# Kernel tuning notes

Hardware: AMD Instinct MI355X
Metric: run time of the kernel (lower is better)

The kernel has to match this reference:

```python
import jax, jax.numpy as jnp
import numpy as np

KERNEL_EPS = 1e-3   # generalized_kernel epsilon (performer)
Z_EPS = 1e-6        # LinearHopfieldCore eps


def _phi(x, proj):
    # generalized_kernel with relu: phi(x) = relu(d^{-0.25} * x @ P^T) + 1e-3
    # x: [B, L, H, D], proj: [M, D] -> [B, L, H, M]
    scale = x.shape[-1] ** -0.25
    return jax.nn.relu(jnp.einsum('blhd,md->blhm', x * scale, proj)) + KERNEL_EPS


def setup_inputs() -> dict:
    key = jax.random.key(0)
    kq, kk, kv, kp = jax.random.split(key, 4)
    B, L, H, D, M = 4, 4096, 16, 64, 256
    return {
        'q': jax.random.normal(kq, (B, L, H, D), dtype=jnp.float32),
        'k': jax.random.normal(kk, (B, L, H, D), dtype=jnp.float32),
        'v': jax.random.normal(kv, (B, L, H, D), dtype=jnp.float32),
        'projection_matrix': jax.random.normal(kp, (M, D), dtype=jnp.float32),
    }


def reference(q, k, v, projection_matrix):
    # Feature maps [B, L, H, M]
    Qf = _phi(q, projection_matrix)
    Kf = _phi(k, projection_matrix)
    # Linear attention (non-causal):
    # KV = sum_s K_s otimes V_s : [B, H, M, E]
    KV = jnp.einsum('bshm,bshe->bhme', Kf, v)
    # Z = 1 / (Q . (sum_s K_s + eps)) : [B, H, L]
    Ksum = jnp.sum(Kf, axis=1) + Z_EPS        # [B, H, M]
    Z = 1.0 / jnp.einsum('blhm,bhm->bhl', Qf, Ksum)
    # out = (Q @ KV) * Z : [B, L, H, E]
    out = jnp.einsum('bhme,blhm,bhl->blhe', KV, Qf, Z)
    return out
```

## Files before the change

kernel.cpp:

```cpp
#include <hip/hip_runtime.h>


#define LL 4096
#define HH 16
#define DD 64
#define EE 64
#define MM 256
#define SCALE 0.35355339059327378f

typedef __attribute__((ext_vector_type(8))) __bf16 bf8v;
typedef __attribute__((ext_vector_type(4))) __bf16 bf4v;
typedef __attribute__((ext_vector_type(4))) float f4v;

__device__ __forceinline__ __bf16 f2bf(float f) {
  union { float f; unsigned u; } x; x.f = f;
  unsigned r = (x.u + 0x7FFFu + ((x.u >> 16) & 1u)) >> 16;
  union { unsigned short s; __bf16 b; } y; y.s = (unsigned short)r;
  return y.b;
}

__device__ __forceinline__ void barrier_lgkm() {
  asm volatile("s_waitcnt lgkmcnt(0)" ::: "memory");
  __builtin_amdgcn_s_barrier();
  asm volatile("" ::: "memory");
}

#define MFMA16(a, b, c) __builtin_amdgcn_mfma_f32_16x16x32_bf16(a, b, c, 0, 0, 0)

#define PKV_ELEMS (8ull * 64 * 64 * 256)
#define PKS_ELEMS (8ull * 64 * 256)
#define KV_ELEMS (64ull * 64 * 256)
#define KS_ELEMS (64ull * 256)
#define WS_PART_BYTES ((PKV_ELEMS + PKS_ELEMS + KV_ELEMS + KS_ELEMS) * 4)
#define WS_ATOMIC_BYTES ((KV_ELEMS + KS_ELEMS) * 4)

#define ARENA_BYTES 72704
#define KT_OFF 0
#define VT_OFF 18432
#define KFT_OFF 35840

__global__ __launch_bounds__(512, 4)
void k1_kv(const float* __restrict__ kin, const float* __restrict__ vin,
           const float* __restrict__ pin,
           float* __restrict__ pkv, float* __restrict__ pks,
           float* __restrict__ kv, float* __restrict__ ks, int partials) {
  __shared__ alignas(16) char arena[ARENA_BYTES];
  __bf16* ktA[2] = {(__bf16*)(arena + KT_OFF), (__bf16*)(arena + KT_OFF) + 64 * 72};
  __bf16* vtA[2] = {(__bf16*)(arena + VT_OFF), (__bf16*)(arena + VT_OFF) + 64 * 68};
  __bf16* kft = (__bf16*)(arena + KFT_OFF);

  const int tid = threadIdx.x;
  const int w = tid >> 6;
  const int lane = tid & 63;
  const int qd = lane >> 4;
  const int nn = lane & 15;
  const int bh = blockIdx.y;
  const int b = bh >> 4, h = bh & 15;
  const int l0 = blockIdx.x * 512;

  const size_t bhbase = (size_t)b * LL * HH * DD + (size_t)h * DD;
  const int r0 = tid >> 4;
  const int c0 = (tid & 15) * 4;

  const float* gk = kin + bhbase + (size_t)(l0 + r0) * (HH * DD) + c0;
  const float* gv = vin + bhbase + (size_t)(l0 + r0) * (HH * DD) + c0;
  const size_t RSTEP = (size_t)32 * HH * DD;
  const size_t TSTEP = (size_t)64 * HH * DD;

  f4v kr[2][2], vr[2][2];
  kr[0][0] = *(const f4v*)gk;          kr[0][1] = *(const f4v*)(gk + RSTEP);
  vr[0][0] = *(const f4v*)gv;          vr[0][1] = *(const f4v*)(gv + RSTEP);
  gk += TSTEP; gv += TSTEP;
  kr[1][0] = *(const f4v*)gk;          kr[1][1] = *(const f4v*)(gk + RSTEP);
  vr[1][0] = *(const f4v*)gv;          vr[1][1] = *(const f4v*)(gv + RSTEP);
  gk += TSTEP; gv += TSTEP;

  bf8v pf[2][2];
#pragma unroll
  for (int mt = 0; mt < 2; ++mt) {
    const float* pr = pin + (size_t)(32 * w + mt * 16 + nn) * DD;
#pragma unroll
    for (int c = 0; c < 2; ++c) {
      bf8v t;
#pragma unroll
      for (int j = 0; j < 8; ++j) t[j] = f2bf(pr[c * 32 + qd * 8 + j] * SCALE);
      pf[mt][c] = t;
    }
  }

  f4v acc[2][4];
#pragma unroll
  for (int i = 0; i < 2; ++i)
#pragma unroll
    for (int j = 0; j < 4; ++j) acc[i][j] = (f4v){0.f, 0.f, 0.f, 0.f};
  float ksum[2] = {0.f, 0.f};

  auto stage = [&](int buf, const f4v* kk, const f4v* vv) {
    __bf16* ktb = ktA[buf];
    __bf16* vtb = vtA[buf];
#pragma unroll
    for (int rr = 0; rr < 2; ++rr) {
      bf4v a, c;
#pragma unroll
      for (int j = 0; j < 4; ++j) { a[j] = f2bf(kk[rr][j]); c[j] = f2bf(vv[rr][j]); }
      *(bf4v*)&ktb[(r0 + 32 * rr) * 72 + c0] = a;
      *(bf4v*)&vtb[(r0 + 32 * rr) * 68 + c0] = c;
    }
  };

  auto gemm12 = [&](int buf) {
    const __bf16* ktb = ktA[buf];
    const __bf16* vtb = vtA[buf];
#pragma unroll
    for (int lt = 0; lt < 4; ++lt) {
      bf8v a0 = *(const bf8v*)&ktb[(lt * 16 + nn) * 72 + qd * 8];
      bf8v a1 = *(const bf8v*)&ktb[(lt * 16 + nn) * 72 + 32 + qd * 8];
#pragma unroll
      for (int mt = 0; mt < 2; ++mt) {
        f4v cc = (f4v){0.f, 0.f, 0.f, 0.f};
        cc = MFMA16(a0, pf[mt][0], cc);
        cc = MFMA16(a1, pf[mt][1], cc);
        bf4v pk4;
#pragma unroll
        for (int r = 0; r < 4; ++r) {
          float ph = fmaxf(cc[r], 0.f) + 1e-3f;
          ksum[mt] += ph;
          pk4[r] = f2bf(ph);
        }
        *(bf4v*)&kft[(32 * w + mt * 16 + nn) * 72 + lt * 16 + qd * 4] = pk4;
      }
    }
#pragma unroll
    for (int c = 0; c < 2; ++c) {
      bf8v af0 = *(const bf8v*)&kft[(32 * w + nn) * 72 + c * 32 + qd * 8];
      bf8v af1 = *(const bf8v*)&kft[(32 * w + 16 + nn) * 72 + c * 32 + qd * 8];
#pragma unroll
      for (int et = 0; et < 4; ++et) {
        bf8v bv;
#pragma unroll
        for (int j = 0; j < 8; ++j) bv[j] = vtb[(c * 32 + qd * 8 + j) * 68 + et * 16 + nn];
        acc[0][et] = MFMA16(af0, bv, acc[0][et]);
        acc[1][et] = MFMA16(af1, bv, acc[1][et]);
      }
    }
  };

  stage(0, kr[0], vr[0]);
  barrier_lgkm();

#pragma unroll
  for (int t = 0; t < 8; ++t) {
    const int cur = t & 1;
    if (t + 2 < 8) {
      kr[cur][0] = *(const f4v*)gk;      kr[cur][1] = *(const f4v*)(gk + RSTEP);
      vr[cur][0] = *(const f4v*)gv;      vr[cur][1] = *(const f4v*)(gv + RSTEP);
      gk += TSTEP; gv += TSTEP;
    }
    gemm12(cur);
    if (t + 1 < 8) {
      stage(cur ^ 1, kr[cur ^ 1], vr[cur ^ 1]);
      barrier_lgkm();
    }
  }

  if (partials) {
    barrier_lgkm();
    float* ep = (float*)arena;
#pragma unroll
    for (int mt = 0; mt < 2; ++mt)
#pragma unroll
      for (int et = 0; et < 4; ++et)
        *(f4v*)&ep[(et * 16 + nn) * 260 + 32 * w + mt * 16 + 4 * qd] = acc[mt][et];
    barrier_lgkm();
    float* dst = pkv + (size_t)(blockIdx.x * 64 + bh) * (64 * 256);
#pragma unroll
    for (int rr = 0; rr < 8; ++rr) {
      int f = tid + 512 * rr;
      int e = f >> 6;
      int m4 = f & 63;
      f4v val = *(const f4v*)&ep[e * 260 + m4 * 4];
      ((f4v*)dst)[f] = val;
    }
#pragma unroll
    for (int mt = 0; mt < 2; ++mt) {
      float s = ksum[mt];
      s += __shfl_xor(s, 16, 64);
      s += __shfl_xor(s, 32, 64);
      if (lane < 16)
        pks[(size_t)(blockIdx.x * 64 + bh) * 256 + 32 * w + mt * 16 + lane] = s;
    }
  } else {
    float* kvb = kv + (size_t)bh * (64 * 256);
#pragma unroll
    for (int mt = 0; mt < 2; ++mt)
#pragma unroll
      for (int et = 0; et < 4; ++et)
#pragma unroll
        for (int r = 0; r < 4; ++r) {
          int m = 32 * w + mt * 16 + 4 * qd + r;
          int e = et * 16 + nn;
          atomicAdd(&kvb[e * 256 + m], acc[mt][et][r]);
        }
#pragma unroll
    for (int mt = 0; mt < 2; ++mt) {
      float s = ksum[mt];
      s += __shfl_xor(s, 16, 64);
      s += __shfl_xor(s, 32, 64);
      if (lane < 16) atomicAdd(&ks[bh * 256 + 32 * w + mt * 16 + lane], s);
    }
  }
}

__global__ __launch_bounds__(256)
void k2_red(const float* __restrict__ pkv, const float* __restrict__ pks,
            float* __restrict__ kv, float* __restrict__ ks) {
  const int idx = blockIdx.x * 256 + threadIdx.x;
  if (idx < 262144) {
    f4v s = (f4v){0.f, 0.f, 0.f, 0.f};
#pragma unroll
    for (int x = 0; x < 8; ++x) s += ((const f4v*)pkv)[(size_t)x * 262144 + idx];
    ((f4v*)kv)[idx] = s;
  } else {
    const int j = idx - 262144;
    f4v s = (f4v){0.f, 0.f, 0.f, 0.f};
#pragma unroll
    for (int x = 0; x < 8; ++x) s += ((const f4v*)pks)[x * 4096 + j];
    ((f4v*)ks)[j] = s;
  }
}

__global__ __launch_bounds__(512, 4)
void k3_out(const float* __restrict__ qin, const float* __restrict__ pin,
            const float* __restrict__ kv, const float* __restrict__ ksm,
            float* __restrict__ out) {
  __shared__ __bf16 qt[2][64 * 72];
  __shared__ __bf16 qf[64 * 264];
  __shared__ float denp[256];
  __shared__ float ksume[256];

  const int tid = threadIdx.x;
  const int w = tid >> 6;
  const int wm = w & 3;
  const int wl = w >> 2;
  const int lane = tid & 63;
  const int qd = lane >> 4;
  const int nn = lane & 15;
  const int bh = blockIdx.y;
  const int b = bh >> 4, h = bh & 15;
  const int l0 = blockIdx.x * 512;
  const int lt0 = 2 * wl;

  const size_t bhbase = (size_t)b * LL * HH * DD + (size_t)h * DD;
  const int r0 = tid >> 4;
  const int c0 = (tid & 15) * 4;

  const float* gq = qin + bhbase + (size_t)(l0 + r0) * (HH * DD) + c0;
  const size_t RSTEP = (size_t)32 * HH * DD;
  const size_t TSTEP = (size_t)64 * HH * DD;

  f4v qr[2][2];
  qr[0][0] = *(const f4v*)gq;  qr[0][1] = *(const f4v*)(gq + RSTEP);
  gq += TSTEP;
  qr[1][0] = *(const f4v*)gq;  qr[1][1] = *(const f4v*)(gq + RSTEP);
  gq += TSTEP;

  bf8v pf[4][2];
#pragma unroll
  for (int mt = 0; mt < 4; ++mt) {
    const float* pr = pin + (size_t)(64 * wm + mt * 16 + nn) * DD;
#pragma unroll
    for (int c = 0; c < 2; ++c) {
      bf8v t;
#pragma unroll
      for (int j = 0; j < 8; ++j) t[j] = f2bf(pr[c * 32 + qd * 8 + j] * SCALE);
      pf[mt][c] = t;
    }
  }

  const float* kvb = kv + (size_t)bh * (64 * 256);
  bf8v kvf[8];
#pragma unroll
  for (int c = 0; c < 8; ++c) {
    const float* src = kvb + (size_t)(16 * wm + nn) * 256 + c * 32 + qd * 8;
    bf8v t;
#pragma unroll
    for (int j = 0; j < 8; ++j) t[j] = f2bf(src[j]);
    kvf[c] = t;
  }

  if (tid < 256) ksume[tid] = ksm[bh * 256 + tid] + 1e-6f;

  auto stage = [&](int buf, const f4v* qq) {
    __bf16* qtb = &qt[buf][0];
#pragma unroll
    for (int rr = 0; rr < 2; ++rr) {
      bf4v a;
#pragma unroll
      for (int j = 0; j < 4; ++j) a[j] = f2bf(qq[rr][j]);
      *(bf4v*)&qtb[(r0 + 32 * rr) * 72 + c0] = a;
    }
  };

  stage(0, qr[0]);
  barrier_lgkm();

#pragma unroll
  for (int t = 0; t < 8; ++t) {
    const int cur = t & 1;
    if (t + 2 < 8) {
      qr[cur][0] = *(const f4v*)gq;  qr[cur][1] = *(const f4v*)(gq + RSTEP);
      gq += TSTEP;
    }

    {
      const __bf16* qtb = &qt[cur][0];
#pragma unroll
      for (int li = 0; li < 2; ++li) {
        const int lt = lt0 + li;
        bf8v b0 = *(const bf8v*)&qtb[(lt * 16 + nn) * 72 + qd * 8];
        bf8v b1 = *(const bf8v*)&qtb[(lt * 16 + nn) * 72 + 32 + qd * 8];
        float dpart = 0.f;
#pragma unroll
        for (int mt = 0; mt < 4; ++mt) {
          f4v cc = (f4v){0.f, 0.f, 0.f, 0.f};
          cc = MFMA16(pf[mt][0], b0, cc);
          cc = MFMA16(pf[mt][1], b1, cc);
          bf4v pk4;
#pragma unroll
          for (int r = 0; r < 4; ++r) {
            float ph = fmaxf(cc[r], 0.f) + 1e-3f;
            dpart += ph * ksume[64 * wm + mt * 16 + 4 * qd + r];
            pk4[r] = f2bf(ph);
          }
          *(bf4v*)&qf[(lt * 16 + nn) * 264 + 64 * wm + mt * 16 + 4 * qd] = pk4;
        }
        dpart += __shfl_xor(dpart, 16, 64);
        dpart += __shfl_xor(dpart, 32, 64);
        if (lane < 16) denp[wm * 64 + lt * 16 + lane] = dpart;
      }
    }
    barrier_lgkm();

#pragma unroll
    for (int li = 0; li < 2; ++li) {
      const int lt = lt0 + li;
      f4v co0 = (f4v){0.f, 0.f, 0.f, 0.f};
      f4v co1 = (f4v){0.f, 0.f, 0.f, 0.f};
#pragma unroll
      for (int c = 0; c < 4; ++c) {
        bf8v afa = *(const bf8v*)&qf[(lt * 16 + nn) * 264 + c * 32 + qd * 8];
        bf8v afb = *(const bf8v*)&qf[(lt * 16 + nn) * 264 + (c + 4) * 32 + qd * 8];
        co0 = MFMA16(afa, kvf[c], co0);
        co1 = MFMA16(afb, kvf[c + 4], co1);
      }
      f4v d0 = *(const f4v*)&denp[0 * 64 + lt * 16 + 4 * qd];
      f4v d1 = *(const f4v*)&denp[1 * 64 + lt * 16 + 4 * qd];
      f4v d2 = *(const f4v*)&denp[2 * 64 + lt * 16 + 4 * qd];
      f4v d3 = *(const f4v*)&denp[3 * 64 + lt * 16 + 4 * qd];
#pragma unroll
      for (int r = 0; r < 4; ++r) {
        int lrel = lt * 16 + 4 * qd + r;
        int labs = l0 + t * 64 + lrel;
        float rden = 1.f / (d0[r] + d1[r] + d2[r] + d3[r]);
        out[((size_t)((size_t)b * LL + labs) * HH + h) * EE + 16 * wm + nn] =
            (co0[r] + co1[r]) * rden;
      }
    }

    if (t + 1 < 8) {
      stage(cur ^ 1, qr[cur ^ 1]);
      barrier_lgkm();
    }
  }
}

extern "C" void kernel_launch(void* const* d_in, const int* in_sizes, int n_in,
                              void* d_out, int out_size, void* d_ws, size_t ws_size,
                              hipStream_t stream) {
  (void)in_sizes; (void)n_in; (void)out_size;
  const float* q = (const float*)d_in[0];
  const float* k = (const float*)d_in[1];
  const float* v = (const float*)d_in[2];
  const float* p = (const float*)d_in[3];
  float* ws = (float*)d_ws;
  float* out = (float*)d_out;

  dim3 grid(8, 64), blk(512);
  if (ws_size >= WS_PART_BYTES) {
    float* pkv = ws;
    float* pks = ws + PKV_ELEMS;
    float* kvp = ws + PKV_ELEMS + PKS_ELEMS;
    float* ksp = kvp + KV_ELEMS;
    k1_kv<<<grid, blk, 0, stream>>>(k, v, p, pkv, pks, nullptr, nullptr, 1);
    k2_red<<<dim3(1040), dim3(256), 0, stream>>>(pkv, pks, kvp, ksp);
    k3_out<<<grid, blk, 0, stream>>>(q, p, kvp, ksp, out);
  } else if (ws_size >= WS_ATOMIC_BYTES) {
    float* kvp = ws;
    float* ksp = ws + KV_ELEMS;
    hipMemsetAsync(d_ws, 0, WS_ATOMIC_BYTES, stream);
    k1_kv<<<grid, blk, 0, stream>>>(k, v, p, nullptr, nullptr, kvp, ksp, 0);
    k3_out<<<grid, blk, 0, stream>>>(q, p, kvp, ksp, out);
  }
}
```

Before: 376.5 us.

## Transpose V in LDS, pad rows to 76, hoist Ksum to registers, restage pipeline

In the KV kernel, V is now stored transposed in shared memory so the B-operand of the second MFMA is one vectorized 16-byte LDS read instead of eight strided scalar reads. Row strides change from 72/68/264 to 76/268 to shift bank-conflict patterns. Staging of the next tile now happens before the gemm with a single barrier per iteration, and the Q kernel keeps Ksum in registers instead of LDS. The custom bf16 rounding is replaced by the native cast, and occupancy hints drop from 4 to 3 blocks because of the larger LDS footprint.

```diff
diff --git a/kernel.cpp b/kernel.cpp
--- a/kernel.cpp
+++ b/kernel.cpp
@@ -12,12 +12,7 @@
 typedef __attribute__((ext_vector_type(4))) __bf16 bf4v;
 typedef __attribute__((ext_vector_type(4))) float f4v;
 
-__device__ __forceinline__ __bf16 f2bf(float f) {
-  union { float f; unsigned u; } x; x.f = f;
-  unsigned r = (x.u + 0x7FFFu + ((x.u >> 16) & 1u)) >> 16;
-  union { unsigned short s; __bf16 b; } y; y.s = (unsigned short)r;
-  return y.b;
-}
+__device__ __forceinline__ __bf16 f2bf(float f) { return (__bf16)f; }
 
 __device__ __forceinline__ void barrier_lgkm() {
   asm volatile("s_waitcnt lgkmcnt(0)" ::: "memory");
@@ -34,19 +29,19 @@
 #define WS_PART_BYTES ((PKV_ELEMS + PKS_ELEMS + KV_ELEMS + KS_ELEMS) * 4)
 #define WS_ATOMIC_BYTES ((KV_ELEMS + KS_ELEMS) * 4)
 
-#define ARENA_BYTES 72704
+#define ARENA_BYTES 77824
 #define KT_OFF 0
-#define VT_OFF 18432
-#define KFT_OFF 35840
-
-__global__ __launch_bounds__(512, 4)
+#define VT_OFF 19456
+#define KFT_OFF 38912
+
+__global__ __launch_bounds__(512, 3)
 void k1_kv(const float* __restrict__ kin, const float* __restrict__ vin,
            const float* __restrict__ pin,
            float* __restrict__ pkv, float* __restrict__ pks,
            float* __restrict__ kv, float* __restrict__ ks, int partials) {
   __shared__ alignas(16) char arena[ARENA_BYTES];
-  __bf16* ktA[2] = {(__bf16*)(arena + KT_OFF), (__bf16*)(arena + KT_OFF) + 64 * 72};
-  __bf16* vtA[2] = {(__bf16*)(arena + VT_OFF), (__bf16*)(arena + VT_OFF) + 64 * 68};
+  __bf16* ktA[2] = {(__bf16*)(arena + KT_OFF), (__bf16*)(arena + KT_OFF) + 64 * 76};
+  __bf16* vtA[2] = {(__bf16*)(arena + VT_OFF), (__bf16*)(arena + VT_OFF) + 64 * 76};
   __bf16* kft = (__bf16*)(arena + KFT_OFF);
 
   const int tid = threadIdx.x;
@@ -67,12 +62,11 @@
   const size_t RSTEP = (size_t)32 * HH * DD;
   const size_t TSTEP = (size_t)64 * HH * DD;
 
-  f4v kr[2][2], vr[2][2];
-  kr[0][0] = *(const f4v*)gk;          kr[0][1] = *(const f4v*)(gk + RSTEP);
-  vr[0][0] = *(const f4v*)gv;          vr[0][1] = *(const f4v*)(gv + RSTEP);
+  f4v kc0 = *(const f4v*)gk, kc1 = *(const f4v*)(gk + RSTEP);
+  f4v vc0 = *(const f4v*)gv, vc1 = *(const f4v*)(gv + RSTEP);
   gk += TSTEP; gv += TSTEP;
-  kr[1][0] = *(const f4v*)gk;          kr[1][1] = *(const f4v*)(gk + RSTEP);
-  vr[1][0] = *(const f4v*)gv;          vr[1][1] = *(const f4v*)(gv + RSTEP);
+  f4v kn0 = *(const f4v*)gk, kn1 = *(const f4v*)(gk + RSTEP);
+  f4v vn0 = *(const f4v*)gv, vn1 = *(const f4v*)(gv + RSTEP);
   gk += TSTEP; gv += TSTEP;
 
   bf8v pf[2][2];
@@ -95,16 +89,18 @@
     for (int j = 0; j < 4; ++j) acc[i][j] = (f4v){0.f, 0.f, 0.f, 0.f};
   float ksum[2] = {0.f, 0.f};
 
-  auto stage = [&](int buf, const f4v* kk, const f4v* vv) {
+  auto stage = [&](int buf, f4v k0, f4v k1, f4v v0, f4v v1) {
     __bf16* ktb = ktA[buf];
     __bf16* vtb = vtA[buf];
-#pragma unroll
-    for (int rr = 0; rr < 2; ++rr) {
-      bf4v a, c;
-#pragma unroll
-      for (int j = 0; j < 4; ++j) { a[j] = f2bf(kk[rr][j]); c[j] = f2bf(vv[rr][j]); }
-      *(bf4v*)&ktb[(r0 + 32 * rr) * 72 + c0] = a;
-      *(bf4v*)&vtb[(r0 + 32 * rr) * 68 + c0] = c;
+    bf4v a0, a1;
+#pragma unroll
+    for (int j = 0; j < 4; ++j) { a0[j] = f2bf(k0[j]); a1[j] = f2bf(k1[j]); }
+    *(bf4v*)&ktb[r0 * 76 + c0] = a0;
+    *(bf4v*)&ktb[(r0 + 32) * 76 + c0] = a1;
+#pragma unroll
+    for (int j = 0; j < 4; ++j) {
+      vtb[(c0 + j) * 76 + r0] = f2bf(v0[j]);
+      vtb[(c0 + j) * 76 + r0 + 32] = f2bf(v1[j]);
     }
   };
 
@@ -113,8 +109,8 @@
     const __bf16* vtb = vtA[buf];
 #pragma unroll
     for (int lt = 0; lt < 4; ++lt) {
-      bf8v a0 = *(const bf8v*)&ktb[(lt * 16 + nn) * 72 + qd * 8];
-      bf8v a1 = *(const bf8v*)&ktb[(lt * 16 + nn) * 72 + 32 + qd * 8];
+      bf8v a0 = *(const bf8v*)&ktb[(lt * 16 + nn) * 76 + qd * 8];
+      bf8v a1 = *(const bf8v*)&ktb[(lt * 16 + nn) * 76 + 32 + qd * 8];
 #pragma unroll
       for (int mt = 0; mt < 2; ++mt) {
         f4v cc = (f4v){0.f, 0.f, 0.f, 0.f};
@@ -127,44 +123,42 @@
           ksum[mt] += ph;
           pk4[r] = f2bf(ph);
         }
-        *(bf4v*)&kft[(32 * w + mt * 16 + nn) * 72 + lt * 16 + qd * 4] = pk4;
+        *(bf4v*)&kft[(32 * w + mt * 16 + nn) * 76 + lt * 16 + qd * 4] = pk4;
       }
     }
 #pragma unroll
     for (int c = 0; c < 2; ++c) {
-      bf8v af0 = *(const bf8v*)&kft[(32 * w + nn) * 72 + c * 32 + qd * 8];
-      bf8v af1 = *(const bf8v*)&kft[(32 * w + 16 + nn) * 72 + c * 32 + qd * 8];
+      bf8v af0 = *(const bf8v*)&kft[(32 * w + nn) * 76 + c * 32 + qd * 8];
+      bf8v af1 = *(const bf8v*)&kft[(32 * w + 16 + nn) * 76 + c * 32 + qd * 8];
 #pragma unroll
       for (int et = 0; et < 4; ++et) {
-        bf8v bv;
-#pragma unroll
-        for (int j = 0; j < 8; ++j) bv[j] = vtb[(c * 32 + qd * 8 + j) * 68 + et * 16 + nn];
+        bf8v bv = *(const bf8v*)&vtb[(et * 16 + nn) * 76 + c * 32 + qd * 8];
         acc[0][et] = MFMA16(af0, bv, acc[0][et]);
         acc[1][et] = MFMA16(af1, bv, acc[1][et]);
       }
     }
   };
 
-  stage(0, kr[0], vr[0]);
+  stage(0, kc0, kc1, vc0, vc1);
   barrier_lgkm();
 
 #pragma unroll
   for (int t = 0; t < 8; ++t) {
     const int cur = t & 1;
-    if (t + 2 < 8) {
-      kr[cur][0] = *(const f4v*)gk;      kr[cur][1] = *(const f4v*)(gk + RSTEP);
-      vr[cur][0] = *(const f4v*)gv;      vr[cur][1] = *(const f4v*)(gv + RSTEP);
-      gk += TSTEP; gv += TSTEP;
+    if (t + 1 < 8) {
+      kc0 = kn0; kc1 = kn1; vc0 = vn0; vc1 = vn1;
+      if (t + 2 < 8) {
+        kn0 = *(const f4v*)gk; kn1 = *(const f4v*)(gk + RSTEP);
+        vn0 = *(const f4v*)gv; vn1 = *(const f4v*)(gv + RSTEP);
+        gk += TSTEP; gv += TSTEP;
+      }
+      stage(cur ^ 1, kc0, kc1, vc0, vc1);
     }
     gemm12(cur);
-    if (t + 1 < 8) {
-      stage(cur ^ 1, kr[cur ^ 1], vr[cur ^ 1]);
-      barrier_lgkm();
-    }
+    barrier_lgkm();
   }
 
   if (partials) {
-    barrier_lgkm();
     float* ep = (float*)arena;
 #pragma unroll
     for (int mt = 0; mt < 2; ++mt)
@@ -229,14 +223,13 @@
   }
 }
 
-__global__ __launch_bounds__(512, 4)
+__global__ __launch_bounds__(512, 3)
 void k3_out(const float* __restrict__ qin, const float* __restrict__ pin,
             const float* __restrict__ kv, const float* __restrict__ ksm,
             float* __restrict__ out) {
-  __shared__ __bf16 qt[2][64 * 72];
-  __shared__ __bf16 qf[64 * 264];
+  __shared__ __bf16 qt[2][64 * 76];
+  __shared__ __bf16 qf[64 * 268];
   __shared__ float denp[256];
-  __shared__ float ksume[256];
 
   const int tid = threadIdx.x;
   const int w = tid >> 6;
@@ -258,10 +251,9 @@
   const size_t RSTEP = (size_t)32 * HH * DD;
   const size_t TSTEP = (size_t)64 * HH * DD;
 
-  f4v qr[2][2];
-  qr[0][0] = *(const f4v*)gq;  qr[0][1] = *(const f4v*)(gq + RSTEP);
+  f4v qc0 = *(const f4v*)gq, qc1 = *(const f4v*)(gq + RSTEP);
   gq += TSTEP;
-  qr[1][0] = *(const f4v*)gq;  qr[1][1] = *(const f4v*)(gq + RSTEP);
+  f4v qn0 = *(const f4v*)gq, qn1 = *(const f4v*)(gq + RSTEP);
   gq += TSTEP;
 
   bf8v pf[4][2];
@@ -288,37 +280,36 @@
     kvf[c] = t;
   }
 
-  if (tid < 256) ksume[tid] = ksm[bh * 256 + tid] + 1e-6f;
-
-  auto stage = [&](int buf, const f4v* qq) {
+  f4v ke[4];
+#pragma unroll
+  for (int mt = 0; mt < 4; ++mt) {
+    f4v t = *(const f4v*)&ksm[bh * 256 + 64 * wm + mt * 16 + 4 * qd];
+    ke[mt] = t + (f4v){1e-6f, 1e-6f, 1e-6f, 1e-6f};
+  }
+
+  auto stage = [&](int buf, f4v q0, f4v q1) {
     __bf16* qtb = &qt[buf][0];
-#pragma unroll
-    for (int rr = 0; rr < 2; ++rr) {
-      bf4v a;
-#pragma unroll
-      for (int j = 0; j < 4; ++j) a[j] = f2bf(qq[rr][j]);
-      *(bf4v*)&qtb[(r0 + 32 * rr) * 72 + c0] = a;
-    }
+    bf4v a0, a1;
+#pragma unroll
+    for (int j = 0; j < 4; ++j) { a0[j] = f2bf(q0[j]); a1[j] = f2bf(q1[j]); }
+    *(bf4v*)&qtb[r0 * 76 + c0] = a0;
+    *(bf4v*)&qtb[(r0 + 32) * 76 + c0] = a1;
   };
 
-  stage(0, qr[0]);
+  stage(0, qc0, qc1);
   barrier_lgkm();
 
 #pragma unroll
   for (int t = 0; t < 8; ++t) {
     const int cur = t & 1;
-    if (t + 2 < 8) {
-      qr[cur][0] = *(const f4v*)gq;  qr[cur][1] = *(const f4v*)(gq + RSTEP);
-      gq += TSTEP;
-    }
 
     {
       const __bf16* qtb = &qt[cur][0];
 #pragma unroll
       for (int li = 0; li < 2; ++li) {
         const int lt = lt0 + li;
-        bf8v b0 = *(const bf8v*)&qtb[(lt * 16 + nn) * 72 + qd * 8];
-        bf8v b1 = *(const bf8v*)&qtb[(lt * 16 + nn) * 72 + 32 + qd * 8];
+        bf8v b0 = *(const bf8v*)&qtb[(lt * 16 + nn) * 76 + qd * 8];
+        bf8v b1 = *(const bf8v*)&qtb[(lt * 16 + nn) * 76 + 32 + qd * 8];
         float dpart = 0.f;
 #pragma unroll
         for (int mt = 0; mt < 4; ++mt) {
@@ -329,10 +320,10 @@
 #pragma unroll
           for (int r = 0; r < 4; ++r) {
             float ph = fmaxf(cc[r], 0.f) + 1e-3f;
-            dpart += ph * ksume[64 * wm + mt * 16 + 4 * qd + r];
+            dpart += ph * ke[mt][r];
             pk4[r] = f2bf(ph);
           }
-          *(bf4v*)&qf[(lt * 16 + nn) * 264 + 64 * wm + mt * 16 + 4 * qd] = pk4;
+          *(bf4v*)&qf[(lt * 16 + nn) * 268 + 64 * wm + mt * 16 + 4 * qd] = pk4;
         }
         dpart += __shfl_xor(dpart, 16, 64);
         dpart += __shfl_xor(dpart, 32, 64);
@@ -348,8 +339,8 @@
       f4v co1 = (f4v){0.f, 0.f, 0.f, 0.f};
 #pragma unroll
       for (int c = 0; c < 4; ++c) {
-        bf8v afa = *(const bf8v*)&qf[(lt * 16 + nn) * 264 + c * 32 + qd * 8];
-        bf8v afb = *(const bf8v*)&qf[(lt * 16 + nn) * 264 + (c + 4) * 32 + qd * 8];
+        bf8v afa = *(const bf8v*)&qf[(lt * 16 + nn) * 268 + c * 32 + qd * 8];
+        bf8v afb = *(const bf8v*)&qf[(lt * 16 + nn) * 268 + (c + 4) * 32 + qd * 8];
         co0 = MFMA16(afa, kvf[c], co0);
         co1 = MFMA16(afb, kvf[c + 4], co1);
       }
@@ -368,7 +359,12 @@
     }
 
     if (t + 1 < 8) {
-      stage(cur ^ 1, qr[cur ^ 1]);
+      qc0 = qn0; qc1 = qn1;
+      if (t + 2 < 8) {
+        qn0 = *(const f4v*)gq; qn1 = *(const f4v*)(gq + RSTEP);
+        gq += TSTEP;
+      }
+      stage(cur ^ 1, qc0, qc1);
       barrier_lgkm();
     }
   }
```

Result: faster. 307.7 us (-18.3%).
